# Optimization experiments

Measured on AMD Instinct MI355X. Metric: run time of the kernel, lower is better.

## Reference

```python
import jax, jax.numpy as jnp
import numpy as np

WIN, SIGMA = 11, 1.5
C1, C2, EPS = 0.01 ** 2, 0.03 ** 2, 1e-8


def _gauss_window(win=WIN, sigma=SIGMA):
    coords = jnp.arange(win, dtype=jnp.float32) - (win - 1) / 2
    g = jnp.exp(-coords ** 2 / (2 * sigma ** 2))
    g = g / g.sum()
    return (g[:, None] * g[None, :])[None, None, :, :]


def setup_inputs() -> dict:
    key = jax.random.key(0)
    k1, k2 = jax.random.split(key)
    N, C, H, W = 32, 1, 512, 512
    x = jax.random.uniform(k1, (N, C, H, W), dtype=jnp.float32)
    y = jax.random.uniform(k2, (N, C, H, W), dtype=jnp.float32)
    w = _gauss_window()
    return {"x": x, "y": y, "w": w}


def _conv(x, w):
    pad = w.shape[-1] // 2
    return jax.lax.conv_general_dilated(
        x, w, window_strides=(1, 1), padding=[(pad, pad), (pad, pad)],
        dimension_numbers=("NCHW", "OIHW", "NCHW"))


def reference(x, y, w):
    w = w.astype(x.dtype)
    n = x.shape[0]
    # One fused conv over all five planes stacked on the batch dim.
    stacked = jnp.concatenate([x, y, x * x, y * y, x * y], axis=0)
    conv = _conv(stacked, w)
    mu_x, mu_y, ex2, ey2, exy = (conv[i * n:(i + 1) * n] for i in range(5))
    mu_x2, mu_y2, mu_xy = mu_x ** 2, mu_y ** 2, mu_x * mu_y
    sig_x2 = ex2 - mu_x2
    sig_y2 = ey2 - mu_y2
    sig_xy = exy - mu_xy
    num = (2 * mu_xy + C1) * (2 * sig_xy + C2)
    den = (mu_x2 + mu_y2 + C1) * (sig_x2 + sig_y2 + C2)
    return jnp.clip(num / (den + EPS), 0.0, 1.0).mean()
```

## Files before the change

kernel.cpp:

```cpp
#include <hip/hip_runtime.h>


typedef float v2f __attribute__((ext_vector_type(2)));
typedef float v4f __attribute__((ext_vector_type(4)));

#define IMG_H 512
#define IMG_W 512
#define NIMG  32
#define NT    256
#define RROWS 26
#define NCHX  20
#define ITERS 36
#define SEGW  144

#define C1F  1.0e-4f
#define C2F  9.0e-4f
#define EPSF 1.0e-8f

static __device__ __forceinline__ v2f pkfma(float s, v2f a, v2f b) {
    v2f sv = {s, s};
    return __builtin_elementwise_fma(sv, a, b);
}

__global__ __launch_bounds__(NT) void ssim_kernel(
    const float* __restrict__ xg, const float* __restrict__ yg,
    const float* __restrict__ wg, float* __restrict__ out)
{
    const int t    = threadIdx.x;
    const int lane = t & 63;
    const int wv   = t >> 6;
    const int chnk = blockIdx.x;
    const int img  = blockIdx.y;
    const int r0   = chnk * RROWS;
    const int C0   = 128 * wv;
    const int cown = C0 + 2 * lane;
    const int c0l  = 2 * lane;

    const float* xb = xg + (size_t)img * (IMG_H * IMG_W);
    const float* yb = yg + (size_t)img * (IMG_H * IMG_W);

    __shared__ alignas(16) v2f seg[4][3][SEGW];
    __shared__ float wredS[4];

    float rs = 0.f;
    if (lane < 11) {
        #pragma unroll
        for (int j = 0; j < 11; ++j) rs += wg[lane * 11 + j];
    }
    float g[11];
    #pragma unroll
    for (int k = 0; k < 11; ++k) {
        int gi = __shfl(__float_as_int(rs), k, 64);
        g[k] = __int_as_float(__builtin_amdgcn_readfirstlane(gi));
    }

    const v2f z2 = {0.f, 0.f};

    const bool isH = (lane < 3) || (lane >= 61);
    const int  hcol = (lane < 3) ? (C0 - 6 + 2 * lane)
                                 : (C0 + 128 + 2 * (lane - 61));
    const int  hidx = (lane < 3) ? (2 * lane) : (134 + 2 * (lane - 61));

    v2f px0, py0, hx0, hy0;
    v2f px1, py1, hx1, hy1;

#define LOADROW(ROW, SUF) do {                                             \
        const int r_ = (ROW);                                              \
        px##SUF = z2; py##SUF = z2; hx##SUF = z2; hy##SUF = z2;            \
        if ((unsigned)r_ < IMG_H) {                                        \
            const float* xr = xb + (size_t)r_ * IMG_W;                     \
            const float* yr = yb + (size_t)r_ * IMG_W;                     \
            px##SUF = *(const v2f*)(xr + cown);                            \
            py##SUF = *(const v2f*)(yr + cown);                            \
            if (isH && (unsigned)hcol < IMG_W) {                           \
                hx##SUF = *(const v2f*)(xr + hcol);                        \
                hy##SUF = *(const v2f*)(yr + hcol);                        \
            }                                                              \
        }                                                                  \
    } while (0)

#define WRITESLOT(SL, SUF) do {                                            \
        const v2f sv_ = px##SUF + py##SUF;               \
        const v2f dv_ = px##SUF - py##SUF;                                 \
        v4f st_ = {sv_.x, dv_.x, sv_.y, dv_.y};                            \
        *(v4f*)&seg[wv][(SL)][6 + c0l] = st_;                              \
        if (isH) {                                                         \
            const v2f hs_ = hx##SUF + hy##SUF;                             \
            const v2f hd_ = hx##SUF - hy##SUF;                             \
            v4f ht_ = {hs_.x, hd_.x, hs_.y, hd_.y};                        \
            *(v4f*)&seg[wv][(SL)][hidx] = ht_;                             \
        }                                                                  \
    } while (0)

    LOADROW(r0 - 5, 0);
    LOADROW(r0 - 4, 1);
    WRITESLOT(0, 0);
    WRITESLOT(1, 1);
    LOADROW(r0 - 3, 0);
    LOADROW(r0 - 2, 1);

    v2f rSD[12][2], rQ[12][2];

    float acc = 0.f;

    #pragma unroll 1
    for (int base = 0; base < ITERS; base += 12) {
        #pragma unroll
        for (int s = 0; s < 12; ++s) {
            const int i = base + s;

            v4f w4r[7];
            #pragma unroll
            for (int m = 0; m < 7; ++m)
                w4r[m] = *(const v4f*)&seg[wv][s % 3][c0l + 2 * m];

            if (i <= ITERS - 3) {
                if (s % 2 == 0) WRITESLOT((s + 2) % 3, 0);
                else            WRITESLOT((s + 2) % 3, 1);
            }

            if (i <= ITERS - 5) {
                if (s % 2 == 0) LOADROW(r0 - 5 + i + 4, 0);
                else            LOADROW(r0 - 5 + i + 4, 1);
            }

            v2f hA = z2, hB = z2, qA = z2, qB = z2;
            #pragma unroll
            for (int m = 0; m < 7; ++m) {
                const v4f w4 = w4r[m];
                const v2f e0 = {w4.x, w4.y};
                const v2f e1 = {w4.z, w4.w};
                {
                    const int j = 2 * m;
                    if (j >= 1) {
                        const v2f f0 = e0 * e0;
                        if (j <= 11) {
                            hA = pkfma(g[j - 1], e0, hA);
                            qA = pkfma(g[j - 1], f0, qA);
                        }
                        if (j >= 2) {
                            hB = pkfma(g[j - 2], e0, hB);
                            qB = pkfma(g[j - 2], f0, qB);
                        }
                    }
                }
                {
                    const int j = 2 * m + 1;
                    if (j <= 12) {
                        const v2f f1 = e1 * e1;
                        if (j <= 11) {
                            hA = pkfma(g[j - 1], e1, hA);
                            qA = pkfma(g[j - 1], f1, qA);
                        }
                        if (j >= 2) {
                            hB = pkfma(g[j - 2], e1, hB);
                            qB = pkfma(g[j - 2], f1, qB);
                        }
                    }
                }
            }
            rSD[s][0] = hA; rSD[s][1] = hB;
            rQ[s][0]  = qA; rQ[s][1]  = qB;

            if (i >= 10) {
                const int orow = r0 + i - 10;
                if (orow < IMG_H) {
                    #pragma unroll
                    for (int cc = 0; cc < 2; ++cc) {
                        v2f mSD = z2, mQ = z2;
                        #pragma unroll
                        for (int j = 0; j < 11; ++j) {
                            const int sl = (s + 2 + j) % 12;
                            mSD = pkfma(g[j], rSD[sl][cc], mSD);
                            mQ  = pkfma(g[j], rQ[sl][cc],  mQ);
                        }
                        const v2f t2 = mSD * mSD;
                        const float a    = 0.5f  * (t2.x + t2.y);
                        const float muxy = 0.25f * (t2.x - t2.y);
                        const float ep   = 0.5f  * (mQ.x + mQ.y);
                        const float eq   = 0.25f * (mQ.x - mQ.y);
                        const float sxy  = eq - muxy;
                        const float ssum = ep - a;
                        const float num  = fmaf(2.f, muxy, C1F) * fmaf(2.f, sxy, C2F);
                        const float den  = (a + C1F) * (ssum + C2F);
                        float v = num * __builtin_amdgcn_rcpf(den + EPSF);
                        acc += fminf(fmaxf(v, 0.f), 1.f);
                    }
                }
            }
        }
    }

    #pragma unroll
    for (int off = 32; off > 0; off >>= 1)
        acc += __shfl_down(acc, off, 64);
    if (lane == 0) wredS[wv] = acc;
    __syncthreads();
    if (t == 0) {
        const float tot = (wredS[0] + wredS[1]) + (wredS[2] + wredS[3]);
        atomicAdd(out, tot * (1.0f / (float)((size_t)NIMG * IMG_H * IMG_W)));
    }
}

extern "C" void kernel_launch(void* const* d_in, const int* in_sizes, int n_in,
                              void* d_out, int out_size, void* d_ws, size_t ws_size,
                              hipStream_t stream) {
    const float* x = (const float*)d_in[0];
    const float* y = (const float*)d_in[1];
    const float* w = (const float*)d_in[2];
    float* out = (float*)d_out;

    hipMemsetAsync(out, 0, sizeof(float), stream);

    dim3 grid(NCHX, NIMG);
    ssim_kernel<<<grid, dim3(NT), 0, stream>>>(x, y, w, out);
}
```

Baseline: 123.6 us.

## Switch SSIM kernel to one column per lane with taller row chunks

Each lane now handles one column instead of two, and a wave covers a 64-column segment. The grid gains a second block per row chunk along x, and each chunk grows from 26 to 38 rows (14 chunks instead of 20). The aim is to cut per-thread register pressure, which the launch-bound minimum-blocks hint also targets, and to amortize the 10-row vertical halo over more output rows. The cost is a larger horizontal halo overhead, since 10 extra columns are now loaded per 64 instead of per 128, plus scalar rather than vector loads.

```diff
diff --git a/kernel.cpp b/kernel.cpp
--- a/kernel.cpp
+++ b/kernel.cpp
@@ -2,16 +2,15 @@
 
 
 typedef float v2f __attribute__((ext_vector_type(2)));
-typedef float v4f __attribute__((ext_vector_type(4)));
 
 #define IMG_H 512
 #define IMG_W 512
 #define NIMG  32
 #define NT    256
-#define RROWS 26
-#define NCHX  20
-#define ITERS 36
-#define SEGW  144
+#define RROWS 38
+#define NCHNK 14
+#define ITERS 48
+#define SLOTW 80
 
 #define C1F  1.0e-4f
 #define C2F  9.0e-4f
@@ -22,24 +21,25 @@
     return __builtin_elementwise_fma(sv, a, b);
 }
 
-__global__ __launch_bounds__(NT) void ssim_kernel(
+__global__ __launch_bounds__(NT, 4) void ssim_kernel(
     const float* __restrict__ xg, const float* __restrict__ yg,
     const float* __restrict__ wg, float* __restrict__ out)
 {
     const int t    = threadIdx.x;
     const int lane = t & 63;
     const int wv   = t >> 6;
-    const int chnk = blockIdx.x;
+    const int bx   = blockIdx.x;
     const int img  = blockIdx.y;
+    const int chnk = bx >> 1;
+    const int seg  = ((bx & 1) << 2) | wv;
     const int r0   = chnk * RROWS;
-    const int C0   = 128 * wv;
-    const int cown = C0 + 2 * lane;
-    const int c0l  = 2 * lane;
+    const int C0   = seg * 64;
+    const int cown = C0 + lane;
 
     const float* xb = xg + (size_t)img * (IMG_H * IMG_W);
     const float* yb = yg + (size_t)img * (IMG_H * IMG_W);
 
-    __shared__ alignas(16) v2f seg[4][3][SEGW];
+    __shared__ alignas(16) v2f seg3[4][3][SLOTW];
     __shared__ float wredS[4];
 
     float rs = 0.f;
@@ -54,41 +54,34 @@
         g[k] = __int_as_float(__builtin_amdgcn_readfirstlane(gi));
     }
 
-    const v2f z2 = {0.f, 0.f};
+    const bool isH  = (lane < 5) || (lane >= 59);
+    const int  hcol = (lane < 5) ? (C0 - 5 + lane) : (C0 + 64 + (lane - 59));
+    const int  hidx = (lane < 5) ? lane : (lane + 10);
 
-    const bool isH = (lane < 3) || (lane >= 61);
-    const int  hcol = (lane < 3) ? (C0 - 6 + 2 * lane)
-                                 : (C0 + 128 + 2 * (lane - 61));
-    const int  hidx = (lane < 3) ? (2 * lane) : (134 + 2 * (lane - 61));
-
-    v2f px0, py0, hx0, hy0;
-    v2f px1, py1, hx1, hy1;
+    float px0, py0, hx0, hy0;
+    float px1, py1, hx1, hy1;
 
 #define LOADROW(ROW, SUF) do {                                             \
         const int r_ = (ROW);                                              \
-        px##SUF = z2; py##SUF = z2; hx##SUF = z2; hy##SUF = z2;            \
+        px##SUF = 0.f; py##SUF = 0.f; hx##SUF = 0.f; hy##SUF = 0.f;        \
         if ((unsigned)r_ < IMG_H) {                                        \
             const float* xr = xb + (size_t)r_ * IMG_W;                     \
             const float* yr = yb + (size_t)r_ * IMG_W;                     \
-            px##SUF = *(const v2f*)(xr + cown);                            \
-            py##SUF = *(const v2f*)(yr + cown);                            \
+            px##SUF = xr[cown];                                            \
+            py##SUF = yr[cown];                                            \
             if (isH && (unsigned)hcol < IMG_W) {                           \
-                hx##SUF = *(const v2f*)(xr + hcol);                        \
-                hy##SUF = *(const v2f*)(yr + hcol);                        \
+                hx##SUF = xr[hcol];                                        \
+                hy##SUF = yr[hcol];                                        \
             }                                                              \
         }                                                                  \
     } while (0)
 
 #define WRITESLOT(SL, SUF) do {                                            \
-        const v2f sv_ = px##SUF + py##SUF;               \
-        const v2f dv_ = px##SUF - py##SUF;                                 \
-        v4f st_ = {sv_.x, dv_.x, sv_.y, dv_.y};                            \
-        *(v4f*)&seg[wv][(SL)][6 + c0l] = st_;                              \
+        v2f sd_ = {px##SUF + py##SUF, px##SUF - py##SUF};                  \
+        seg3[wv][(SL)][5 + lane] = sd_;                                    \
         if (isH) {                                                         \
-            const v2f hs_ = hx##SUF + hy##SUF;                             \
-            const v2f hd_ = hx##SUF - hy##SUF;                             \
-            v4f ht_ = {hs_.x, hd_.x, hs_.y, hd_.y};                        \
-            *(v4f*)&seg[wv][(SL)][hidx] = ht_;                             \
+            v2f hsd_ = {hx##SUF + hy##SUF, hx##SUF - hy##SUF};             \
+            seg3[wv][(SL)][hidx] = hsd_;                                   \
         }                                                                  \
     } while (0)
 
@@ -99,7 +92,7 @@
     LOADROW(r0 - 3, 0);
     LOADROW(r0 - 2, 1);
 
-    v2f rSD[12][2], rQ[12][2];
+    v2f rSD[12], rQ[12];
 
     float acc = 0.f;
 
@@ -109,10 +102,10 @@
         for (int s = 0; s < 12; ++s) {
             const int i = base + s;
 
-            v4f w4r[7];
+            v2f e[11];
             #pragma unroll
-            for (int m = 0; m < 7; ++m)
-                w4r[m] = *(const v4f*)&seg[wv][s % 3][c0l + 2 * m];
+            for (int j = 0; j < 11; ++j)
+                e[j] = seg3[wv][s % 3][lane + j];
 
             if (i <= ITERS - 3) {
                 if (s % 2 == 0) WRITESLOT((s + 2) % 3, 0);
@@ -124,68 +117,37 @@
                 else            LOADROW(r0 - 5 + i + 4, 1);
             }
 
-            v2f hA = z2, hB = z2, qA = z2, qB = z2;
+            v2f hSD = {0.f, 0.f}, hQ = {0.f, 0.f};
             #pragma unroll
-            for (int m = 0; m < 7; ++m) {
-                const v4f w4 = w4r[m];
-                const v2f e0 = {w4.x, w4.y};
-                const v2f e1 = {w4.z, w4.w};
-                {
-                    const int j = 2 * m;
-                    if (j >= 1) {
-                        const v2f f0 = e0 * e0;
-                        if (j <= 11) {
-                            hA = pkfma(g[j - 1], e0, hA);
-                            qA = pkfma(g[j - 1], f0, qA);
-                        }
-                        if (j >= 2) {
-                            hB = pkfma(g[j - 2], e0, hB);
-                            qB = pkfma(g[j - 2], f0, qB);
-                        }
-                    }
-                }
-                {
-                    const int j = 2 * m + 1;
-                    if (j <= 12) {
-                        const v2f f1 = e1 * e1;
-                        if (j <= 11) {
-                            hA = pkfma(g[j - 1], e1, hA);
-                            qA = pkfma(g[j - 1], f1, qA);
-                        }
-                        if (j >= 2) {
-                            hB = pkfma(g[j - 2], e1, hB);
-                            qB = pkfma(g[j - 2], f1, qB);
-                        }
-                    }
-                }
+            for (int j = 0; j < 11; ++j) {
+                const v2f f = e[j] * e[j];
+                hSD = pkfma(g[j], e[j], hSD);
+                hQ  = pkfma(g[j], f,    hQ);
             }
-            rSD[s][0] = hA; rSD[s][1] = hB;
-            rQ[s][0]  = qA; rQ[s][1]  = qB;
+            rSD[s] = hSD;
+            rQ[s]  = hQ;
 
             if (i >= 10) {
                 const int orow = r0 + i - 10;
                 if (orow < IMG_H) {
+                    v2f mSD = {0.f, 0.f}, mQ = {0.f, 0.f};
                     #pragma unroll
-                    for (int cc = 0; cc < 2; ++cc) {
-                        v2f mSD = z2, mQ = z2;
-                        #pragma unroll
-                        for (int j = 0; j < 11; ++j) {
-                            const int sl = (s + 2 + j) % 12;
-                            mSD = pkfma(g[j], rSD[sl][cc], mSD);
-                            mQ  = pkfma(g[j], rQ[sl][cc],  mQ);
-                        }
-                        const v2f t2 = mSD * mSD;
-                        const float a    = 0.5f  * (t2.x + t2.y);
-                        const float muxy = 0.25f * (t2.x - t2.y);
-                        const float ep   = 0.5f  * (mQ.x + mQ.y);
-                        const float eq   = 0.25f * (mQ.x - mQ.y);
-                        const float sxy  = eq - muxy;
-                        const float ssum = ep - a;
-                        const float num  = fmaf(2.f, muxy, C1F) * fmaf(2.f, sxy, C2F);
-                        const float den  = (a + C1F) * (ssum + C2F);
-                        float v = num * __builtin_amdgcn_rcpf(den + EPSF);
-                        acc += fminf(fmaxf(v, 0.f), 1.f);
+                    for (int j = 0; j < 11; ++j) {
+                        const int sl = (s + 2 + j) % 12;
+                        mSD = pkfma(g[j], rSD[sl], mSD);
+                        mQ  = pkfma(g[j], rQ[sl],  mQ);
                     }
+                    const v2f t2 = mSD * mSD;
+                    const float a    = 0.5f  * (t2.x + t2.y);
+                    const float muxy = 0.25f * (t2.x - t2.y);
+                    const float ep   = 0.5f  * (mQ.x + mQ.y);
+                    const float eq   = 0.25f * (mQ.x - mQ.y);
+                    const float sxy  = eq - muxy;
+                    const float ssum = ep - a;
+                    const float num  = fmaf(2.f, muxy, C1F) * fmaf(2.f, sxy, C2F);
+                    const float den  = (a + C1F) * (ssum + C2F);
+                    float v = num * __builtin_amdgcn_rcpf(den + EPSF);
+                    acc += fminf(fmaxf(v, 0.f), 1.f);
                 }
             }
         }
@@ -212,6 +174,6 @@
 
     hipMemsetAsync(out, 0, sizeof(float), stream);
 
-    dim3 grid(NCHX, NIMG);
+    dim3 grid(NCHNK * 2, NIMG);
     ssim_kernel<<<grid, dim3(NT), 0, stream>>>(x, y, w, out);
 }
```

Result: faster. 120.6 us (-2.4%).
